# Performance work log

Hardware: AMD Instinct MI355X
Metric: run time of the kernel (lower is better)

Reference implementation:

```python
import jax, jax.numpy as jnp
import numpy as np

B, T, D, E, F, K = 1, 8192, 1024, 8, 4096, 2
CAP_FACTOR = 1.25
AUX_COEFF = 0.01


def setup_inputs() -> dict:
    key = jax.random.key(0)
    k0, k1, k2, k3, k4 = jax.random.split(key, 5)
    x = jax.random.normal(k0, (B, T, D), dtype=jnp.float32)
    Wr = jax.random.normal(k1, (E, D), dtype=jnp.float32) * 0.01  # router, std=0.01 per init
    s = 0.02
    Wg = jax.random.normal(k2, (E, F, D), dtype=jnp.float32) * s  # gate_proj per expert
    Wu = jax.random.normal(k3, (E, F, D), dtype=jnp.float32) * s  # up_proj per expert
    Wd = jax.random.normal(k4, (E, D, F), dtype=jnp.float32) * s  # down_proj per expert
    return {"x": x, "Wr": Wr, "Wg": Wg, "Wu": Wu, "Wd": Wd}


def reference(x, Wr, Wg, Wu, Wd):
    b, t, d = x.shape
    N = b * t
    capacity = max(int(t * K * CAP_FACTOR / E), 1)  # static, matches compute_capacity
    x_flat = x.reshape(N, d)

    # --- router ---
    logits = x_flat @ Wr.T                              # (N, E)
    probs = jax.nn.softmax(logits, axis=-1)
    topw_raw, topi = jax.lax.top_k(probs, K)            # (N, K)
    topw = topw_raw / (topw_raw.sum(-1, keepdims=True) + 1e-9)

    # --- dispatch order: slot-major (slot 0 over all tokens, then slot 1, ...) ---
    flat_e = topi.T.reshape(-1)                         # (K*N,) expert id per assignment
    flat_w = topw.T.reshape(-1)                         # (K*N,)
    tok = jnp.tile(jnp.arange(N), K)                    # (K*N,) token id per assignment

    oh = jax.nn.one_hot(flat_e, E, dtype=jnp.int32)     # (K*N, E)
    rank = (jnp.cumsum(oh, axis=0) - oh)[jnp.arange(K * N), flat_e]  # arrival rank per expert
    accepted = rank < capacity                          # dispatch_mask (slot-major flat)
    pos = jnp.where(accepted, rank, 0)
    dest = flat_e * capacity + pos                      # slot in flattened capacity buffer
    acc_f = accepted.astype(x.dtype)[:, None]

    # scatter tokens into capacity buffers (dropped tokens add zeros)
    buf = jnp.zeros((E * capacity, d), x.dtype).at[dest].add(x_flat[tok] * acc_f)
    expert_in = buf.reshape(E, capacity, d)

    # --- per-expert SwiGLU FFN (batched grouped GEMM) ---
    gate = jax.nn.silu(jnp.einsum('ecd,efd->ecf', expert_in, Wg))
    up = jnp.einsum('ecd,efd->ecf', expert_in, Wu)
    expert_out = jnp.einsum('ecf,edf->ecd', gate * up, Wd).reshape(E * capacity, d)

    # --- weighted combine back to token positions ---
    contrib = flat_w[:, None] * acc_f * expert_out[dest]
    out_flat = jnp.zeros((N, d), x.dtype).at[tok].add(contrib)
    output = out_flat.reshape(b, t, d)

    # --- load-balance aux loss ---
    counts = jnp.zeros(E, x.dtype).at[flat_e].add(accepted.astype(x.dtype))
    total = jnp.maximum(accepted.sum().astype(x.dtype), 1.0)
    f_i = counts / total
    P_i = probs.mean(0)
    aux_loss = AUX_COEFF * E * jnp.sum(f_i * P_i)
    return output, aux_loss
```

## Files before the change

### kernel.cpp

```cpp
#include <hip/hip_runtime.h>
#include <hip/hip_bf16.h>

#define N_TOK 8192
#define DIM   1024
#define NEXP  8
#define FF    4096
#define CAP   2560
#define NASSIGN (N_TOK * 2)

typedef __bf16 bf16;
typedef __bf16 bf16x8 __attribute__((ext_vector_type(8)));
typedef __bf16 bf16x4v __attribute__((ext_vector_type(4)));
typedef float  f32x4  __attribute__((ext_vector_type(4)));

__device__ __forceinline__ void gl2lds16(const bf16* g, bf16* l) {
    __builtin_amdgcn_global_load_lds(
        (const __attribute__((address_space(1))) unsigned int*)g,
        (__attribute__((address_space(3))) unsigned int*)l,
        16, 0, 0);
}

template <int NT, int AST, int BST, int BG1, int BG2>
__device__ __forceinline__ void gemm256_2ph(
    const bf16* __restrict__ pA, const bf16* __restrict__ pB,
    f32x4 acc[8][4], int wave, int lane)
{
    __shared__ bf16 As[2 * 256 * 64];
    __shared__ bf16 Bs[2 * 256 * 64];

    const int wm = wave >> 2, wn = wave & 3;
    const int r16 = lane & 15, c16 = lane >> 4;
    const int wbase = wave * 8 * 64;

    auto STAGE = [&](int kt) {
        const int b = kt & 1;
        const bf16* a  = pA + (size_t)kt * 64;
        const bf16* bb = pB + (size_t)kt * 64;
#pragma unroll
        for (int g = 0; g < 4; ++g)
            gl2lds16(a + (size_t)g * 64 * AST,
                     &As[b * (256 * 64) + g * (64 * 64) + wbase]);
#pragma unroll
        for (int g = 0; g < 4; ++g)
            gl2lds16(bb + (size_t)((g & 1) * BG1 + (g >> 1) * BG2) * BST,
                     &Bs[b * (256 * 64) + g * (64 * 64) + wbase]);
    };

    STAGE(0);
    asm volatile("s_waitcnt vmcnt(0)" ::: "memory");
    __builtin_amdgcn_sched_barrier(0);
    __builtin_amdgcn_s_barrier();
    __builtin_amdgcn_sched_barrier(0);

    for (int kt = 0; kt < NT; ++kt) {
        if (kt + 1 < NT) STAGE(kt + 1);
        const bf16* Asb = &As[(kt & 1) * (256 * 64)];
        const bf16* Bsb = &Bs[(kt & 1) * (256 * 64)];

        bf16x8 bfr[4][2];
#pragma unroll
        for (int nh = 0; nh < 2; ++nh)
#pragma unroll
            for (int np = 0; np < 2; ++np)
#pragma unroll
                for (int kk = 0; kk < 2; ++kk) {
                    int rl = nh * 128 + wn * 32 + np * 16 + r16;
                    int phys = (kk * 4 + c16) ^ (rl & 7);
                    bfr[nh * 2 + np][kk] = *(const bf16x8*)&Bsb[rl * 64 + phys * 8];
                }
#pragma unroll
        for (int mh = 0; mh < 2; ++mh) {
            bf16x8 af[4][2];
#pragma unroll
            for (int mm = 0; mm < 4; ++mm)
#pragma unroll
                for (int kk = 0; kk < 2; ++kk) {
                    int row = wm * 128 + mh * 64 + mm * 16 + r16;
                    int phys = (kk * 4 + c16) ^ (row & 7);
                    af[mm][kk] = *(const bf16x8*)&Asb[row * 64 + phys * 8];
                }
            __builtin_amdgcn_s_setprio(1);
#pragma unroll
            for (int mm = 0; mm < 4; ++mm)
#pragma unroll
                for (int nf = 0; nf < 4; ++nf)
#pragma unroll
                    for (int kk = 0; kk < 2; ++kk)
                        acc[mh * 4 + mm][nf] =
                            __builtin_amdgcn_mfma_f32_16x16x32_bf16(
                                af[mm][kk], bfr[nf][kk], acc[mh * 4 + mm][nf], 0, 0, 0);
            __builtin_amdgcn_s_setprio(0);
        }

        asm volatile("s_waitcnt vmcnt(0)" ::: "memory");
        __builtin_amdgcn_sched_barrier(0);
        __builtin_amdgcn_s_barrier();
        __builtin_amdgcn_sched_barrier(0);
    }
}

__global__ __launch_bounds__(256) void cvt_bf16_kernel(const float* __restrict__ in,
                                                       bf16* __restrict__ out, int n) {
    int stride = gridDim.x * blockDim.x * 8;
    for (int i = (blockIdx.x * blockDim.x + threadIdx.x) * 8; i < n; i += stride) {
        float4 a = *(const float4*)(in + i);
        float4 b = *(const float4*)(in + i + 4);
        bf16x8 o;
        o[0] = (bf16)a.x; o[1] = (bf16)a.y; o[2] = (bf16)a.z; o[3] = (bf16)a.w;
        o[4] = (bf16)b.x; o[5] = (bf16)b.y; o[6] = (bf16)b.z; o[7] = (bf16)b.w;
        *(bf16x8*)(out + i) = o;
    }
}

__global__ __launch_bounds__(256) void router_kernel(const float* __restrict__ x,
                                                     const float* __restrict__ Wr,
                                                     float* __restrict__ probs,
                                                     int* __restrict__ topi,
                                                     float* __restrict__ topw) {
    int wave = threadIdx.x >> 6;
    int lane = threadIdx.x & 63;
    int t = blockIdx.x * 4 + wave;
    const float* xr = x + (size_t)t * DIM;

    double acc[NEXP];
#pragma unroll
    for (int e = 0; e < NEXP; ++e) acc[e] = 0.0;
    for (int i = lane; i < DIM; i += 64) {
        double xv = (double)xr[i];
#pragma unroll
        for (int e = 0; e < NEXP; ++e) acc[e] += xv * (double)Wr[e * DIM + i];
    }
#pragma unroll
    for (int e = 0; e < NEXP; ++e) {
        double v = acc[e];
        for (int off = 32; off > 0; off >>= 1) v += __shfl_down(v, off, 64);
        acc[e] = v;
    }
    if (lane == 0) {
        double mx = acc[0];
        for (int e = 1; e < NEXP; ++e) if (acc[e] > mx) mx = acc[e];
        double p[NEXP], s = 0.0;
        for (int e = 0; e < NEXP; ++e) { p[e] = exp(acc[e] - mx); s += p[e]; }
        float pf[NEXP];
        for (int e = 0; e < NEXP; ++e) { pf[e] = (float)(p[e] / s); probs[t * NEXP + e] = pf[e]; }
        int e1 = 0;
        for (int e = 1; e < NEXP; ++e) if (acc[e] > acc[e1]) e1 = e;
        int e2 = -1;
        for (int e = 0; e < NEXP; ++e) {
            if (e == e1) continue;
            if (e2 < 0 || acc[e] > acc[e2]) e2 = e;
        }
        float w1 = pf[e1], w2 = pf[e2];
        float inv = 1.0f / (w1 + w2 + 1e-9f);
        topi[t * 2 + 0] = e1; topi[t * 2 + 1] = e2;
        topw[t * 2 + 0] = w1 * inv; topw[t * 2 + 1] = w2 * inv;
    }
}

__global__ __launch_bounds__(64) void rank_kernel(const int* __restrict__ topi,
                                                  int* __restrict__ dest,
                                                  int* __restrict__ accf,
                                                  int* __restrict__ counts) {
    int e = blockIdx.x;
    int lane = threadIdx.x;
    const int per = NASSIGN / 64;
    int base = lane * per;
    int cnt = 0;
    for (int i = 0; i < per; ++i) {
        int j = base + i;
        int t = j & (N_TOK - 1), s = j >> 13;
        if (topi[t * 2 + s] == e) cnt++;
    }
    int sum = cnt;
    for (int off = 1; off < 64; off <<= 1) {
        int v = __shfl_up(sum, off, 64);
        if (lane >= off) sum += v;
    }
    int r = sum - cnt;
    int total = __shfl(sum, 63, 64);
    for (int i = 0; i < per; ++i) {
        int j = base + i;
        int t = j & (N_TOK - 1), s = j >> 13;
        if (topi[t * 2 + s] == e) {
            int acc = (r < CAP) ? 1 : 0;
            dest[j] = e * CAP + (acc ? r : 0);
            accf[j] = acc;
            r++;
        }
    }
    if (lane == 63) counts[e] = (total < CAP) ? total : CAP;
}

__global__ __launch_bounds__(256) void gather_kernel(const float* __restrict__ x,
                                                     const int* __restrict__ dest,
                                                     const int* __restrict__ accf,
                                                     bf16* __restrict__ Xe) {
    int j = blockIdx.x;
    if (!accf[j]) return;
    int t = j & (N_TOK - 1);
    int d0 = threadIdx.x * 4;
    float4 v = *(const float4*)(x + (size_t)t * DIM + d0);
    union { bf16 h[4]; uint2 u; } tmp;
    tmp.h[0] = (bf16)v.x; tmp.h[1] = (bf16)v.y; tmp.h[2] = (bf16)v.z; tmp.h[3] = (bf16)v.w;
    *(uint2*)(Xe + (size_t)dest[j] * DIM + d0) = tmp.u;
}

__global__ __launch_bounds__(512, 2) void gateup_kernel(const bf16* __restrict__ Xe,
                                                        const bf16* __restrict__ Wg,
                                                        const bf16* __restrict__ Wu,
                                                        bf16* __restrict__ hbuf) {
    const int lin = blockIdx.x + 10 * (blockIdx.y + 32 * blockIdx.z);
    const int e   = lin & 7;
    const int rem = lin >> 3;
    const int m0  = (rem % 10) * 256;
    const int n0f = (rem / 10) * 128;
    const int tid = threadIdx.x, lane = tid & 63, wave = tid >> 6;
    const int wm = wave >> 2, wn = wave & 3;
    const int r16 = lane & 15, c16 = lane >> 4;

    const int l   = wave * 8 + (lane >> 3);
    const int csw = ((lane & 7) ^ (lane >> 3)) * 8;
    const bf16* pA = Xe + (size_t)e * CAP * DIM + (size_t)(m0 + l) * DIM + csw;
    const int T = (l >> 4) & 1, wnl = l >> 5, r16l = l & 15;
    const bf16* pB = (T ? Wu : Wg) + (size_t)e * FF * DIM
                   + (size_t)(n0f + wnl * 32 + r16l) * DIM + csw;

    f32x4 acc[8][4] = {};
    gemm256_2ph<DIM / 64, DIM, DIM, 64, 16>(pA, pB, acc, wave, lane);

    bf16* hp = hbuf + (size_t)e * CAP * FF;
#pragma unroll
    for (int m = 0; m < 8; ++m)
#pragma unroll
        for (int cg = 0; cg < 2; ++cg)
#pragma unroll
            for (int j = 0; j < 4; ++j) {
                float g = acc[m][cg * 2 + 0][j];
                float u = acc[m][cg * 2 + 1][j];
                float h = (g / (1.f + __expf(-g))) * u;
                int gr = m0 + wm * 128 + m * 16 + c16 * 4 + j;
                int gc = n0f + wn * 32 + cg * 16 + r16;
                hp[(size_t)gr * FF + gc] = (bf16)h;
            }
}

__global__ __launch_bounds__(512, 2) void down_kernel(const bf16* __restrict__ hbuf,
                                                      const bf16* __restrict__ Wd,
                                                      bf16* __restrict__ eo) {
    const int lin = blockIdx.x + 10 * (blockIdx.y + 4 * blockIdx.z);
    const int xcd = lin & 7, pos = lin >> 3;
    const int zc  = xcd * 2 + pos / 40;
    const int e = zc >> 1, kh = zc & 1;
    const int rem40 = pos % 40;
    const int m0 = (rem40 % 10) * 256;
    const int n0 = (rem40 / 10) * 256;
    const int tid = threadIdx.x, lane = tid & 63, wave = tid >> 6;
    const int wm = wave >> 2, wn = wave & 3;
    const int r16 = lane & 15, c16 = lane >> 4;

    const int l   = wave * 8 + (lane >> 3);
    const int csw = ((lane & 7) ^ (lane >> 3)) * 8;
    const bf16* pA = hbuf + (size_t)e * CAP * FF + (size_t)(m0 + l) * FF
                   + kh * (FF / 2) + csw;
    const int nlow = (l >> 4) & 1, wnl = l >> 5, r16l = l & 15;
    const bf16* pB = Wd + (size_t)e * DIM * FF
                   + (size_t)(n0 + wnl * 64 + nlow * 16 + r16l) * FF
                   + kh * (FF / 2) + csw;

    f32x4 acc[8][4] = {};
    gemm256_2ph<FF / 128, FF, FF, 128, 32>(pA, pB, acc, wave, lane);

    bf16* op = eo + (size_t)kh * NEXP * CAP * DIM + (size_t)e * CAP * DIM;
#pragma unroll
    for (int m = 0; m < 8; ++m)
#pragma unroll
        for (int n = 0; n < 4; ++n)
#pragma unroll
            for (int j = 0; j < 4; ++j) {
                int gr = m0 + wm * 128 + m * 16 + c16 * 4 + j;
                int gc = n0 + wn * 64 + n * 16 + r16;
                op[(size_t)gr * DIM + gc] = (bf16)acc[m][n][j];
            }
}

__global__ __launch_bounds__(256) void combine_kernel(const bf16* __restrict__ eo,
                                                      const int* __restrict__ dest,
                                                      const int* __restrict__ accf,
                                                      const float* __restrict__ topw,
                                                      float* __restrict__ out) {
    int t = blockIdx.x;
    float w0 = accf[t] ? topw[t * 2 + 0] : 0.f;
    float w1 = accf[N_TOK + t] ? topw[t * 2 + 1] : 0.f;
    size_t off1 = (size_t)NEXP * CAP * DIM;
    const bf16* a0 = eo + (size_t)dest[t] * DIM;
    const bf16* b0 = eo + (size_t)dest[N_TOK + t] * DIM;
    int d = threadIdx.x * 4;
    bf16x4v a00 = *(const bf16x4v*)(a0 + d);
    bf16x4v a01 = *(const bf16x4v*)(a0 + off1 + d);
    bf16x4v b00 = *(const bf16x4v*)(b0 + d);
    bf16x4v b01 = *(const bf16x4v*)(b0 + off1 + d);
    float4 o;
    o.x = w0 * ((float)a00[0] + (float)a01[0]) + w1 * ((float)b00[0] + (float)b01[0]);
    o.y = w0 * ((float)a00[1] + (float)a01[1]) + w1 * ((float)b00[1] + (float)b01[1]);
    o.z = w0 * ((float)a00[2] + (float)a01[2]) + w1 * ((float)b00[2] + (float)b01[2]);
    o.w = w0 * ((float)a00[3] + (float)a01[3]) + w1 * ((float)b00[3] + (float)b01[3]);
    *(float4*)(out + (size_t)t * DIM + d) = o;
}

__global__ __launch_bounds__(256) void aux_kernel(const float* __restrict__ probs,
                                                  const int* __restrict__ counts,
                                                  float* __restrict__ out_aux) {
    __shared__ float sm[256][NEXP];
    float loc[NEXP];
#pragma unroll
    for (int e = 0; e < NEXP; ++e) loc[e] = 0.f;
    for (int t = threadIdx.x; t < N_TOK; t += 256)
#pragma unroll
        for (int e = 0; e < NEXP; ++e) loc[e] += probs[t * NEXP + e];
#pragma unroll
    for (int e = 0; e < NEXP; ++e) sm[threadIdx.x][e] = loc[e];
    __syncthreads();
    for (int s = 128; s > 0; s >>= 1) {
        if (threadIdx.x < s)
#pragma unroll
            for (int e = 0; e < NEXP; ++e) sm[threadIdx.x][e] += sm[threadIdx.x + s][e];
        __syncthreads();
    }
    if (threadIdx.x == 0) {
        int tot = 0;
        for (int e = 0; e < NEXP; ++e) tot += counts[e];
        float totf = tot > 0 ? (float)tot : 1.f;
        float aux = 0.f;
        for (int e = 0; e < NEXP; ++e)
            aux += ((float)counts[e] / totf) * (sm[0][e] / (float)N_TOK);
        out_aux[0] = 0.01f * (float)NEXP * aux;
    }
}

extern "C" void kernel_launch(void* const* d_in, const int* in_sizes, int n_in,
                              void* d_out, int out_size, void* d_ws, size_t ws_size,
                              hipStream_t stream) {
    const float* x  = (const float*)d_in[0];
    const float* Wr = (const float*)d_in[1];
    const float* Wg = (const float*)d_in[2];
    const float* Wu = (const float*)d_in[3];
    const float* Wd = (const float*)d_in[4];
    float* out = (float*)d_out;

    char* ws = (char*)d_ws;
    size_t off = 0;
    auto alloc = [&](size_t bytes) -> void* {
        void* p = ws + off;
        off += (bytes + 255) & ~(size_t)255;
        return p;
    };
    const size_t NW = (size_t)NEXP * FF * DIM;
    bf16*  Wg_bf = (bf16*)alloc(NW * sizeof(bf16));
    bf16*  Wu_bf = (bf16*)alloc(NW * sizeof(bf16));
    bf16*  Wd_bf = (bf16*)alloc(NW * sizeof(bf16));
    bf16*  Xe    = (bf16*)alloc((size_t)NEXP * CAP * DIM * sizeof(bf16));
    bf16*  hbuf  = (bf16*)alloc((size_t)NEXP * CAP * FF * sizeof(bf16));
    bf16*  eo    = (bf16*)alloc((size_t)2 * NEXP * CAP * DIM * sizeof(bf16));
    float* probs = (float*)alloc((size_t)N_TOK * NEXP * sizeof(float));
    int*   topi  = (int*)alloc((size_t)N_TOK * 2 * sizeof(int));
    float* topw  = (float*)alloc((size_t)N_TOK * 2 * sizeof(float));
    int*   dst   = (int*)alloc((size_t)NASSIGN * sizeof(int));
    int*   accf  = (int*)alloc((size_t)NASSIGN * sizeof(int));
    int*   cnts  = (int*)alloc(NEXP * sizeof(int));

    cvt_bf16_kernel<<<2048, 256, 0, stream>>>(Wg, Wg_bf, (int)NW);
    cvt_bf16_kernel<<<2048, 256, 0, stream>>>(Wu, Wu_bf, (int)NW);
    cvt_bf16_kernel<<<2048, 256, 0, stream>>>(Wd, Wd_bf, (int)NW);
    router_kernel<<<N_TOK / 4, 256, 0, stream>>>(x, Wr, probs, topi, topw);
    rank_kernel<<<NEXP, 64, 0, stream>>>(topi, dst, accf, cnts);
    gather_kernel<<<NASSIGN, 256, 0, stream>>>(x, dst, accf, Xe);
    gateup_kernel<<<dim3(CAP / 256, FF / 128, NEXP), 512, 0, stream>>>(Xe, Wg_bf, Wu_bf, hbuf);
    down_kernel<<<dim3(CAP / 256, DIM / 256, NEXP * 2), 512, 0, stream>>>(hbuf, Wd_bf, eo);
    combine_kernel<<<N_TOK, 256, 0, stream>>>(eo, dst, accf, topw, out);
    aux_kernel<<<1, 256, 0, stream>>>(probs, cnts, out + (size_t)N_TOK * DIM);
}
```

Baseline: 853.0 us.

## Make expert GEMMs persistent with cross-tile prefetch and split-K four for down

The gate/up and down GEMM kernels become persistent: 256 blocks each loop over several tiles, and the first K-slice of the next tile is prefetched during the last K-step of the current one. This hides the prologue load and the tail effect of many short blocks. The down projection now splits K four ways instead of two, so combine sums four partial bf16 outputs. The partial-output buffer reuses the no-longer-needed Wg_bf workspace to save memory. The cost is more partial traffic in combine and a fixed per-block work assignment.

```diff
diff --git a/kernel.cpp b/kernel.cpp
--- a/kernel.cpp
+++ b/kernel.cpp
@@ -7,6 +7,7 @@
 #define FF    4096
 #define CAP   2560
 #define NASSIGN (N_TOK * 2)
+#define EOSL  ((size_t)NEXP * CAP * DIM)
 
 typedef __bf16 bf16;
 typedef __bf16 bf16x8 __attribute__((ext_vector_type(8)));
@@ -20,10 +21,9 @@
         16, 0, 0);
 }
 
-template <int NT, int AST, int BST, int BG1, int BG2>
-__device__ __forceinline__ void gemm256_2ph(
-    const bf16* __restrict__ pA, const bf16* __restrict__ pB,
-    f32x4 acc[8][4], int wave, int lane)
+template <int NT, int AST, int BST, int BG1, int BG2, class UnitFn, class EpiFn>
+__device__ __forceinline__ void gemm256_persist(
+    int nunits, UnitFn unit, EpiFn epi, int wave, int lane)
 {
     __shared__ bf16 As[2 * 256 * 64];
     __shared__ bf16 Bs[2 * 256 * 64];
@@ -32,70 +32,82 @@
     const int r16 = lane & 15, c16 = lane >> 4;
     const int wbase = wave * 8 * 64;
 
-    auto STAGE = [&](int kt) {
-        const int b = kt & 1;
-        const bf16* a  = pA + (size_t)kt * 64;
-        const bf16* bb = pB + (size_t)kt * 64;
+    auto STAGE = [&](const bf16* a, const bf16* bb, int buf) {
 #pragma unroll
         for (int g = 0; g < 4; ++g)
             gl2lds16(a + (size_t)g * 64 * AST,
-                     &As[b * (256 * 64) + g * (64 * 64) + wbase]);
+                     &As[buf * (256 * 64) + g * (64 * 64) + wbase]);
 #pragma unroll
         for (int g = 0; g < 4; ++g)
             gl2lds16(bb + (size_t)((g & 1) * BG1 + (g >> 1) * BG2) * BST,
-                     &Bs[b * (256 * 64) + g * (64 * 64) + wbase]);
-    };
-
-    STAGE(0);
+                     &Bs[buf * (256 * 64) + g * (64 * 64) + wbase]);
+    };
+
+    const bf16 *pA, *pB;
+    unit(0, pA, pB);
+    STAGE(pA, pB, 0);
     asm volatile("s_waitcnt vmcnt(0)" ::: "memory");
     __builtin_amdgcn_sched_barrier(0);
     __builtin_amdgcn_s_barrier();
     __builtin_amdgcn_sched_barrier(0);
 
-    for (int kt = 0; kt < NT; ++kt) {
-        if (kt + 1 < NT) STAGE(kt + 1);
-        const bf16* Asb = &As[(kt & 1) * (256 * 64)];
-        const bf16* Bsb = &Bs[(kt & 1) * (256 * 64)];
-
-        bf16x8 bfr[4][2];
-#pragma unroll
-        for (int nh = 0; nh < 2; ++nh)
-#pragma unroll
-            for (int np = 0; np < 2; ++np)
-#pragma unroll
-                for (int kk = 0; kk < 2; ++kk) {
-                    int rl = nh * 128 + wn * 32 + np * 16 + r16;
-                    int phys = (kk * 4 + c16) ^ (rl & 7);
-                    bfr[nh * 2 + np][kk] = *(const bf16x8*)&Bsb[rl * 64 + phys * 8];
-                }
-#pragma unroll
-        for (int mh = 0; mh < 2; ++mh) {
-            bf16x8 af[4][2];
-#pragma unroll
-            for (int mm = 0; mm < 4; ++mm)
-#pragma unroll
-                for (int kk = 0; kk < 2; ++kk) {
-                    int row = wm * 128 + mh * 64 + mm * 16 + r16;
-                    int phys = (kk * 4 + c16) ^ (row & 7);
-                    af[mm][kk] = *(const bf16x8*)&Asb[row * 64 + phys * 8];
-                }
-            __builtin_amdgcn_s_setprio(1);
-#pragma unroll
-            for (int mm = 0; mm < 4; ++mm)
-#pragma unroll
-                for (int nf = 0; nf < 4; ++nf)
-#pragma unroll
-                    for (int kk = 0; kk < 2; ++kk)
-                        acc[mh * 4 + mm][nf] =
-                            __builtin_amdgcn_mfma_f32_16x16x32_bf16(
-                                af[mm][kk], bfr[nf][kk], acc[mh * 4 + mm][nf], 0, 0, 0);
-            __builtin_amdgcn_s_setprio(0);
+    for (int u = 0; u < nunits; ++u) {
+        const bf16 *pAn = pA, *pBn = pB;
+        const bool more = (u + 1 < nunits);
+        if (more) unit(u + 1, pAn, pBn);
+
+        f32x4 acc[8][4] = {};
+        for (int kt = 0; kt < NT; ++kt) {
+            if (kt + 1 < NT)
+                STAGE(pA + (size_t)(kt + 1) * 64, pB + (size_t)(kt + 1) * 64, (kt + 1) & 1);
+            else if (more)
+                STAGE(pAn, pBn, 0);
+
+            const bf16* Asb = &As[(kt & 1) * (256 * 64)];
+            const bf16* Bsb = &Bs[(kt & 1) * (256 * 64)];
+
+            bf16x8 bfr[4][2];
+#pragma unroll
+            for (int nh = 0; nh < 2; ++nh)
+#pragma unroll
+                for (int np = 0; np < 2; ++np)
+#pragma unroll
+                    for (int kk = 0; kk < 2; ++kk) {
+                        int rl = nh * 128 + wn * 32 + np * 16 + r16;
+                        int phys = (kk * 4 + c16) ^ (rl & 7);
+                        bfr[nh * 2 + np][kk] = *(const bf16x8*)&Bsb[rl * 64 + phys * 8];
+                    }
+#pragma unroll
+            for (int mh = 0; mh < 2; ++mh) {
+                bf16x8 af[4][2];
+#pragma unroll
+                for (int mm = 0; mm < 4; ++mm)
+#pragma unroll
+                    for (int kk = 0; kk < 2; ++kk) {
+                        int row = wm * 128 + mh * 64 + mm * 16 + r16;
+                        int phys = (kk * 4 + c16) ^ (row & 7);
+                        af[mm][kk] = *(const bf16x8*)&Asb[row * 64 + phys * 8];
+                    }
+                __builtin_amdgcn_s_setprio(1);
+#pragma unroll
+                for (int mm = 0; mm < 4; ++mm)
+#pragma unroll
+                    for (int nf = 0; nf < 4; ++nf)
+#pragma unroll
+                        for (int kk = 0; kk < 2; ++kk)
+                            acc[mh * 4 + mm][nf] =
+                                __builtin_amdgcn_mfma_f32_16x16x32_bf16(
+                                    af[mm][kk], bfr[nf][kk], acc[mh * 4 + mm][nf], 0, 0, 0);
+                __builtin_amdgcn_s_setprio(0);
+            }
+
+            asm volatile("s_waitcnt vmcnt(0)" ::: "memory");
+            __builtin_amdgcn_sched_barrier(0);
+            __builtin_amdgcn_s_barrier();
+            __builtin_amdgcn_sched_barrier(0);
         }
-
-        asm volatile("s_waitcnt vmcnt(0)" ::: "memory");
-        __builtin_amdgcn_sched_barrier(0);
-        __builtin_amdgcn_s_barrier();
-        __builtin_amdgcn_sched_barrier(0);
+        epi(u, acc);
+        pA = pAn; pB = pBn;
     }
 }
 
@@ -209,78 +221,87 @@
                                                         const bf16* __restrict__ Wg,
                                                         const bf16* __restrict__ Wu,
                                                         bf16* __restrict__ hbuf) {
-    const int lin = blockIdx.x + 10 * (blockIdx.y + 32 * blockIdx.z);
-    const int e   = lin & 7;
-    const int rem = lin >> 3;
-    const int m0  = (rem % 10) * 256;
-    const int n0f = (rem / 10) * 128;
+    const int b = blockIdx.x;
+    const int e = b & 7, r = b >> 3;
     const int tid = threadIdx.x, lane = tid & 63, wave = tid >> 6;
     const int wm = wave >> 2, wn = wave & 3;
     const int r16 = lane & 15, c16 = lane >> 4;
 
     const int l   = wave * 8 + (lane >> 3);
     const int csw = ((lane & 7) ^ (lane >> 3)) * 8;
-    const bf16* pA = Xe + (size_t)e * CAP * DIM + (size_t)(m0 + l) * DIM + csw;
     const int T = (l >> 4) & 1, wnl = l >> 5, r16l = l & 15;
-    const bf16* pB = (T ? Wu : Wg) + (size_t)e * FF * DIM
-                   + (size_t)(n0f + wnl * 32 + r16l) * DIM + csw;
-
-    f32x4 acc[8][4] = {};
-    gemm256_2ph<DIM / 64, DIM, DIM, 64, 16>(pA, pB, acc, wave, lane);
-
+    const bf16* XeE = Xe + (size_t)e * CAP * DIM + (size_t)l * DIM + csw;
+    const bf16* WE  = (T ? Wu : Wg) + (size_t)e * FF * DIM
+                    + (size_t)(wnl * 32 + r16l) * DIM + csw;
     bf16* hp = hbuf + (size_t)e * CAP * FF;
-#pragma unroll
-    for (int m = 0; m < 8; ++m)
-#pragma unroll
-        for (int cg = 0; cg < 2; ++cg)
-#pragma unroll
-            for (int j = 0; j < 4; ++j) {
-                float g = acc[m][cg * 2 + 0][j];
-                float u = acc[m][cg * 2 + 1][j];
-                float h = (g / (1.f + __expf(-g))) * u;
-                int gr = m0 + wm * 128 + m * 16 + c16 * 4 + j;
-                int gc = n0f + wn * 32 + cg * 16 + r16;
-                hp[(size_t)gr * FF + gc] = (bf16)h;
-            }
+
+    auto unit = [&](int u, const bf16*& pA, const bf16*& pB) {
+        int g = u * 32 + r;
+        int m = g % 10, n = g / 10;
+        pA = XeE + (size_t)(m * 256) * DIM;
+        pB = WE + (size_t)(n * 128) * DIM;
+    };
+    auto epi = [&](int u, f32x4 (&acc)[8][4]) {
+        int g = u * 32 + r;
+        int m0 = (g % 10) * 256, n0f = (g / 10) * 128;
+#pragma unroll
+        for (int m = 0; m < 8; ++m)
+#pragma unroll
+            for (int cg = 0; cg < 2; ++cg)
+#pragma unroll
+                for (int j = 0; j < 4; ++j) {
+                    float gg = acc[m][cg * 2 + 0][j];
+                    float uu = acc[m][cg * 2 + 1][j];
+                    float h = (gg / (1.f + __expf(-gg))) * uu;
+                    int gr = m0 + wm * 128 + m * 16 + c16 * 4 + j;
+                    int gc = n0f + wn * 32 + cg * 16 + r16;
+                    hp[(size_t)gr * FF + gc] = (bf16)h;
+                }
+    };
+    gemm256_persist<DIM / 64, DIM, DIM, 64, 16>(10, unit, epi, wave, lane);
 }
 
 __global__ __launch_bounds__(512, 2) void down_kernel(const bf16* __restrict__ hbuf,
                                                       const bf16* __restrict__ Wd,
                                                       bf16* __restrict__ eo) {
-    const int lin = blockIdx.x + 10 * (blockIdx.y + 4 * blockIdx.z);
-    const int xcd = lin & 7, pos = lin >> 3;
-    const int zc  = xcd * 2 + pos / 40;
-    const int e = zc >> 1, kh = zc & 1;
-    const int rem40 = pos % 40;
-    const int m0 = (rem40 % 10) * 256;
-    const int n0 = (rem40 / 10) * 256;
+    const int b = blockIdx.x;
+    const int e = b & 7, r = b >> 3;
     const int tid = threadIdx.x, lane = tid & 63, wave = tid >> 6;
     const int wm = wave >> 2, wn = wave & 3;
     const int r16 = lane & 15, c16 = lane >> 4;
 
     const int l   = wave * 8 + (lane >> 3);
     const int csw = ((lane & 7) ^ (lane >> 3)) * 8;
-    const bf16* pA = hbuf + (size_t)e * CAP * FF + (size_t)(m0 + l) * FF
-                   + kh * (FF / 2) + csw;
     const int nlow = (l >> 4) & 1, wnl = l >> 5, r16l = l & 15;
-    const bf16* pB = Wd + (size_t)e * DIM * FF
-                   + (size_t)(n0 + wnl * 64 + nlow * 16 + r16l) * FF
-                   + kh * (FF / 2) + csw;
-
-    f32x4 acc[8][4] = {};
-    gemm256_2ph<FF / 128, FF, FF, 128, 32>(pA, pB, acc, wave, lane);
-
-    bf16* op = eo + (size_t)kh * NEXP * CAP * DIM + (size_t)e * CAP * DIM;
-#pragma unroll
-    for (int m = 0; m < 8; ++m)
-#pragma unroll
-        for (int n = 0; n < 4; ++n)
-#pragma unroll
-            for (int j = 0; j < 4; ++j) {
-                int gr = m0 + wm * 128 + m * 16 + c16 * 4 + j;
-                int gc = n0 + wn * 64 + n * 16 + r16;
-                op[(size_t)gr * DIM + gc] = (bf16)acc[m][n][j];
-            }
+    const bf16* hb  = hbuf + (size_t)e * CAP * FF + (size_t)l * FF + csw;
+    const bf16* WdE = Wd + (size_t)e * DIM * FF
+                    + (size_t)(wnl * 64 + nlow * 16 + r16l) * FF + csw;
+    bf16* eoE = eo + (size_t)e * CAP * DIM;
+
+    auto unit = [&](int u, const bf16*& pA, const bf16*& pB) {
+        int g = u * 32 + r;
+        int m = g % 10, pn = g / 10;
+        int kh = pn >> 2, n = pn & 3;
+        pA = hb + (size_t)(m * 256) * FF + kh * (FF / 4);
+        pB = WdE + (size_t)(n * 256) * FF + kh * (FF / 4);
+    };
+    auto epi = [&](int u, f32x4 (&acc)[8][4]) {
+        int g = u * 32 + r;
+        int m0 = (g % 10) * 256, pn = g / 10;
+        int kh = pn >> 2, n0 = (pn & 3) * 256;
+        bf16* op = eoE + (size_t)kh * EOSL;
+#pragma unroll
+        for (int m = 0; m < 8; ++m)
+#pragma unroll
+            for (int nf = 0; nf < 4; ++nf)
+#pragma unroll
+                for (int j = 0; j < 4; ++j) {
+                    int gr = m0 + wm * 128 + m * 16 + c16 * 4 + j;
+                    int gc = n0 + wn * 64 + nf * 16 + r16;
+                    op[(size_t)gr * DIM + gc] = (bf16)acc[m][nf][j];
+                }
+    };
+    gemm256_persist<(FF / 4) / 64, FF, FF, 128, 32>(5, unit, epi, wave, lane);
 }
 
 __global__ __launch_bounds__(256) void combine_kernel(const bf16* __restrict__ eo,
@@ -291,19 +312,22 @@
     int t = blockIdx.x;
     float w0 = accf[t] ? topw[t * 2 + 0] : 0.f;
     float w1 = accf[N_TOK + t] ? topw[t * 2 + 1] : 0.f;
-    size_t off1 = (size_t)NEXP * CAP * DIM;
     const bf16* a0 = eo + (size_t)dest[t] * DIM;
     const bf16* b0 = eo + (size_t)dest[N_TOK + t] * DIM;
     int d = threadIdx.x * 4;
-    bf16x4v a00 = *(const bf16x4v*)(a0 + d);
-    bf16x4v a01 = *(const bf16x4v*)(a0 + off1 + d);
-    bf16x4v b00 = *(const bf16x4v*)(b0 + d);
-    bf16x4v b01 = *(const bf16x4v*)(b0 + off1 + d);
+    float ax = 0, ay = 0, az = 0, aw = 0, bx = 0, by = 0, bz = 0, bw = 0;
+#pragma unroll
+    for (int s4 = 0; s4 < 4; ++s4) {
+        bf16x4v a = *(const bf16x4v*)(a0 + (size_t)s4 * EOSL + d);
+        bf16x4v bb = *(const bf16x4v*)(b0 + (size_t)s4 * EOSL + d);
+        ax += (float)a[0]; ay += (float)a[1]; az += (float)a[2]; aw += (float)a[3];
+        bx += (float)bb[0]; by += (float)bb[1]; bz += (float)bb[2]; bw += (float)bb[3];
+    }
     float4 o;
-    o.x = w0 * ((float)a00[0] + (float)a01[0]) + w1 * ((float)b00[0] + (float)b01[0]);
-    o.y = w0 * ((float)a00[1] + (float)a01[1]) + w1 * ((float)b00[1] + (float)b01[1]);
-    o.z = w0 * ((float)a00[2] + (float)a01[2]) + w1 * ((float)b00[2] + (float)b01[2]);
-    o.w = w0 * ((float)a00[3] + (float)a01[3]) + w1 * ((float)b00[3] + (float)b01[3]);
+    o.x = w0 * ax + w1 * bx;
+    o.y = w0 * ay + w1 * by;
+    o.z = w0 * az + w1 * bz;
+    o.w = w0 * aw + w1 * bw;
     *(float4*)(out + (size_t)t * DIM + d) = o;
 }
 
@@ -355,18 +379,18 @@
         return p;
     };
     const size_t NW = (size_t)NEXP * FF * DIM;
+    bf16*  Wd_bf = (bf16*)alloc(NW * sizeof(bf16));
     bf16*  Wg_bf = (bf16*)alloc(NW * sizeof(bf16));
     bf16*  Wu_bf = (bf16*)alloc(NW * sizeof(bf16));
-    bf16*  Wd_bf = (bf16*)alloc(NW * sizeof(bf16));
     bf16*  Xe    = (bf16*)alloc((size_t)NEXP * CAP * DIM * sizeof(bf16));
     bf16*  hbuf  = (bf16*)alloc((size_t)NEXP * CAP * FF * sizeof(bf16));
-    bf16*  eo    = (bf16*)alloc((size_t)2 * NEXP * CAP * DIM * sizeof(bf16));
     float* probs = (float*)alloc((size_t)N_TOK * NEXP * sizeof(float));
     int*   topi  = (int*)alloc((size_t)N_TOK * 2 * sizeof(int));
     float* topw  = (float*)alloc((size_t)N_TOK * 2 * sizeof(float));
     int*   dst   = (int*)alloc((size_t)NASSIGN * sizeof(int));
     int*   accf  = (int*)alloc((size_t)NASSIGN * sizeof(int));
     int*   cnts  = (int*)alloc(NEXP * sizeof(int));
+    bf16*  eo    = Wg_bf;
 
     cvt_bf16_kernel<<<2048, 256, 0, stream>>>(Wg, Wg_bf, (int)NW);
     cvt_bf16_kernel<<<2048, 256, 0, stream>>>(Wu, Wu_bf, (int)NW);
@@ -374,8 +398,8 @@
     router_kernel<<<N_TOK / 4, 256, 0, stream>>>(x, Wr, probs, topi, topw);
     rank_kernel<<<NEXP, 64, 0, stream>>>(topi, dst, accf, cnts);
     gather_kernel<<<NASSIGN, 256, 0, stream>>>(x, dst, accf, Xe);
-    gateup_kernel<<<dim3(CAP / 256, FF / 128, NEXP), 512, 0, stream>>>(Xe, Wg_bf, Wu_bf, hbuf);
-    down_kernel<<<dim3(CAP / 256, DIM / 256, NEXP * 2), 512, 0, stream>>>(hbuf, Wd_bf, eo);
+    gateup_kernel<<<256, 512, 0, stream>>>(Xe, Wg_bf, Wu_bf, hbuf);
+    down_kernel<<<256, 512, 0, stream>>>(hbuf, Wd_bf, eo);
     combine_kernel<<<N_TOK, 256, 0, stream>>>(eo, dst, accf, topw, out);
     aux_kernel<<<1, 256, 0, stream>>>(probs, cnts, out + (size_t)N_TOK * DIM);
 }
```

New measurement: 830.4 us. 1.03x faster.
